# Performance work log

Hardware: AMD Instinct MI355X
Metric: run time of the kernel (lower is better)

The kernel has to match this reference:

```python
import jax, jax.numpy as jnp
import numpy as np

HID = 10  # hidden_dim


def conv1x1(x, w, b=None):
    # x: [N,C,H,W], w: [O,C] -> [N,O,H,W]
    y = jnp.einsum('oc,nchw->nohw', w, x)
    if b is not None:
        y = y + b[None, :, None, None]
    return y


def gconv1x1(x, w, b=None):
    # grouped 1x1 conv. x: [N,G*ipg,H,W], w: [G,opg,ipg]
    N, C, H, W = x.shape
    G, opg, ipg = w.shape
    xg = x.reshape(N, G, ipg, H, W)
    y = jnp.einsum('goi,ngihw->ngohw', w, xg).reshape(N, G * opg, H, W)
    if b is not None:
        y = y + b[None, :, None, None]
    return y


def _decomp(h_fea, xf, xh, att_w, att_b, w):
    # Decomposition: spatial attention from (fea, xf, xh), gate xf, project.
    att = jax.nn.sigmoid(conv1x1(jnp.concatenate([h_fea, xf, xh], axis=1), att_w, att_b))
    xfh = jax.nn.relu(conv1x1(xf * att, w))
    return xfh, att


def _comp(parts, xh, att_w, att_b, w):
    # Composition: parts [P,N,HID,H,W]; grouped per-part attention then fuse with xh.
    ca = jax.nn.sigmoid(jnp.einsum('pc,pnchw->pnhw', att_w[:, 0], parts) + att_b[:, None, None, None])
    msg = (parts * ca[:, :, None]).sum(0)  # [N,HID,H,W]
    return jax.nn.relu(conv1x1(jnp.concatenate([xh, msg], axis=1), w))


def _update(xh, m0, m1, m2, gate_w, gate_b, cand_w):
    # conv_Update: gated residual update from summed messages.
    cat = jnp.concatenate([xh, m0 + m1 + m2], axis=1)
    g = jax.nn.sigmoid(conv1x1(cat, gate_w, gate_b))
    cand = jax.nn.relu(conv1x1(cat, cand_w))
    return xh * (1.0 - g) + cand * g


def half_graph(h_fea, xh_u, xh_l, xf, xp, pdp_w1, pdp_w2, att_w, att_b,
               compU_att_w, compU_att_b, compU_w,
               compL_att_w, compL_att_b, compL_w,
               decU_att_w, decU_att_b, decU_w,
               decL_att_w, decL_att_b, decL_w,
               updU_gate_w, updU_gate_b, updU_cand_w,
               updL_gate_w, updL_gate_b, updL_cand_w):
    # Part_Dependency: shared trunk then grouped conv -> (dp_u, dp_l)
    t = jax.nn.relu(conv1x1(jnp.concatenate([h_fea, xh_u, xh_l], axis=1), pdp_w1))
    dp = jax.nn.relu(gconv1x1(t, pdp_w2))
    dp_u, dp_l = dp[:, :HID], dp[:, HID:]
    # grouped sigmoid attention over the two half nodes
    a = jax.nn.sigmoid(gconv1x1(jnp.concatenate([xh_u, xh_l], axis=1), att_w, att_b))
    ag_u, ag_l = a[:, 0:1], a[:, 1:2]
    # upper half node
    xphu = _comp(xp[0:4], xh_u, compU_att_w, compU_att_b, compU_w)
    xlh = dp_l * ag_l + xh_u * ag_u  # Pair_Part_Dependency (lower -> upper)
    xfhu, att_u = _decomp(h_fea, xf, xh_u, decU_att_w, decU_att_b, decU_w)
    xh_u_new = _update(xh_u, xphu, xlh, xfhu, updU_gate_w, updU_gate_b, updU_cand_w)
    # lower half node
    xphl = _comp(xp[4:6], xh_l, compL_att_w, compL_att_b, compL_w)
    xuh = dp_u * ag_u + xh_l * ag_l  # Pair_Part_Dependency (upper -> lower)
    xfhl, att_l = _decomp(h_fea, xf, xh_l, decL_att_w, decL_att_b, decL_w)
    xh_l_new = _update(xh_l, xphl, xuh, xfhl, updL_gate_w, updL_gate_b, updL_cand_w)
    return xh_u_new, xh_l_new, att_u, att_l


def setup_inputs() -> dict:
    key = jax.random.key(0)
    N, C, H, W = 8, 256, 128, 128
    ks = jax.random.split(key, 32)
    s = 0.05
    inp = {
        'h_fea': jax.random.normal(ks[0], (N, C, H, W), jnp.float32),
        'xh_u': jax.random.normal(ks[1], (N, HID, H, W), jnp.float32),
        'xh_l': jax.random.normal(ks[2], (N, HID, H, W), jnp.float32),
        'xf': jax.random.normal(ks[3], (N, HID, H, W), jnp.float32),
        'xp': jax.random.normal(ks[4], (6, N, HID, H, W), jnp.float32),
        'pdp_w1': jax.random.normal(ks[5], (2 * HID, C + 2 * HID), jnp.float32) * s,
        'pdp_w2': jax.random.normal(ks[6], (2, HID, HID), jnp.float32) * s,
        'att_w': jax.random.normal(ks[7], (2, 1, HID), jnp.float32) * s,
        'att_b': jnp.zeros((2,), jnp.float32),
        'compU_att_w': jax.random.normal(ks[8], (4, 1, HID), jnp.float32) * s,
        'compU_att_b': jnp.zeros((4,), jnp.float32),
        'compU_w': jax.random.normal(ks[9], (HID, 2 * HID), jnp.float32) * s,
        'compL_att_w': jax.random.normal(ks[10], (2, 1, HID), jnp.float32) * s,
        'compL_att_b': jnp.zeros((2,), jnp.float32),
        'compL_w': jax.random.normal(ks[11], (HID, 2 * HID), jnp.float32) * s,
        'decU_att_w': jax.random.normal(ks[12], (1, C + 2 * HID), jnp.float32) * s,
        'decU_att_b': jnp.zeros((1,), jnp.float32),
        'decU_w': jax.random.normal(ks[13], (HID, HID), jnp.float32) * s,
        'decL_att_w': jax.random.normal(ks[14], (1, C + 2 * HID), jnp.float32) * s,
        'decL_att_b': jnp.zeros((1,), jnp.float32),
        'decL_w': jax.random.normal(ks[15], (HID, HID), jnp.float32) * s,
        'updU_gate_w': jax.random.normal(ks[16], (HID, 2 * HID), jnp.float32) * s,
        'updU_gate_b': jnp.zeros((HID,), jnp.float32),
        'updU_cand_w': jax.random.normal(ks[17], (HID, 2 * HID), jnp.float32) * s,
        'updL_gate_w': jax.random.normal(ks[18], (HID, 2 * HID), jnp.float32) * s,
        'updL_gate_b': jnp.zeros((HID,), jnp.float32),
        'updL_cand_w': jax.random.normal(ks[19], (HID, 2 * HID), jnp.float32) * s,
    }
    return inp


def reference(h_fea, xh_u, xh_l, xf, xp, pdp_w1, pdp_w2, att_w, att_b,
              compU_att_w, compU_att_b, compU_w,
              compL_att_w, compL_att_b, compL_w,
              decU_att_w, decU_att_b, decU_w,
              decL_att_w, decL_att_b, decL_w,
              updU_gate_w, updU_gate_b, updU_cand_w,
              updL_gate_w, updL_gate_b, updL_cand_w):
    return half_graph(h_fea, xh_u, xh_l, xf, xp, pdp_w1, pdp_w2, att_w, att_b,
                      compU_att_w, compU_att_b, compU_w,
                      compL_att_w, compL_att_b, compL_w,
                      decU_att_w, decU_att_b, decU_w,
                      decL_att_w, decL_att_b, decL_w,
                      updU_gate_w, updU_gate_b, updU_cand_w,
                      updL_gate_w, updL_gate_b, updL_cand_w)
```

## Files before the change

kernel.cpp:

```cpp
#include <hip/hip_runtime.h>
#include <stdint.h>

typedef unsigned int   u32;
typedef unsigned short u16;

#define HW 16384

typedef __attribute__((ext_vector_type(8)))  _Float16 half8;
typedef __attribute__((ext_vector_type(16))) float    f32x16;

__device__ __forceinline__ float sigm(float x) { return 1.f / (1.f + __expf(-x)); }


__global__ __launch_bounds__(256) void prep_apack(
    const float* __restrict__ pdp_w1, const float* __restrict__ dU_aw,
    const float* __restrict__ dL_aw, _Float16* __restrict__ apack)
{
    int idx = blockIdx.x * 256 + threadIdx.x;
    int s = idx >> 9, rem = idx & 511, l = rem >> 3, j = rem & 7;
    int o = l & 31, kh = l >> 5;
    int k = s * 16 + kh * 8 + j;
    float wv = 0.f;
    if (o < 20)       wv = pdp_w1[o * 276 + k];
    else if (o == 20) wv = dU_aw[k];
    else if (o == 21) wv = dL_aw[k];
    _Float16 h = (_Float16)wv;
    apack[idx]        = h;
    apack[8192 + idx] = (_Float16)(wv - (float)h);
}

__global__ __launch_bounds__(256, 4) void half_graph_fused(
    const float* __restrict__ hf,  const float* __restrict__ xhu, const float* __restrict__ xhl,
    const float* __restrict__ xfg, const float* __restrict__ xpg,
    const float* __restrict__ pdp_w1, const float* __restrict__ pdp_w2,
    const float* __restrict__ att_w,  const float* __restrict__ att_b,
    const float* __restrict__ cU_aw, const float* __restrict__ cU_ab, const float* __restrict__ cU_w,
    const float* __restrict__ cL_aw, const float* __restrict__ cL_ab, const float* __restrict__ cL_w,
    const float* __restrict__ dU_aw, const float* __restrict__ dU_ab, const float* __restrict__ dU_w,
    const float* __restrict__ dL_aw, const float* __restrict__ dL_ab, const float* __restrict__ dL_w,
    const float* __restrict__ uU_gw, const float* __restrict__ uU_gb, const float* __restrict__ uU_cw,
    const float* __restrict__ uL_gw, const float* __restrict__ uL_gb, const float* __restrict__ uL_cw,
    const _Float16* __restrict__ apack,
    float* __restrict__ out)
{
    const int tid    = threadIdx.x;
    const int pxbase = blockIdx.x * 128;
    const int n      = pxbase >> 14;
    const int hwbase = pxbase & 16383;

    __shared__ float sacc[22][128];

    {
        const int l   = tid & 63;
        const int w   = tid >> 6;
        const int col = l & 31;
        const int kh  = l >> 5;
        const float* bp = hf + ((size_t)n * 256 + kh * 8) * HW + (hwbase + w * 32 + col);
        const half8* ah  = (const half8*)apack;
        const half8* al8 = ah + 1024;
        f32x16 acc = {};
        #pragma unroll 2
        for (int s = 0; s < 16; ++s) {
            half8 A_h = ah[s * 64 + l];
            half8 A_l = al8[s * 64 + l];
            float x[8];
            #pragma unroll
            for (int j = 0; j < 8; ++j) x[j] = bp[(size_t)(s * 16 + j) * HW];
            half8 B_h, B_l;
            #pragma unroll
            for (int j = 0; j < 8; ++j) {
                _Float16 h = (_Float16)x[j];
                B_h[j] = h;
                B_l[j] = (_Float16)(x[j] - (float)h);
            }
            acc = __builtin_amdgcn_mfma_f32_32x32x16_f16(A_h, B_h, acc, 0, 0, 0);
            acc = __builtin_amdgcn_mfma_f32_32x32x16_f16(A_h, B_l, acc, 0, 0, 0);
            acc = __builtin_amdgcn_mfma_f32_32x32x16_f16(A_l, B_h, acc, 0, 0, 0);
        }
        const int ccol = w * 32 + col;
        #pragma unroll
        for (int reg = 0; reg < 12; ++reg) {
            const int r = (reg & 3) + 8 * (reg >> 2) + 4 * kh;
            if (r < 22) sacc[r][ccol] = acc[reg];
        }
    }

    const int q    = tid & 127;
    const int role = tid >> 7;
    const int hw   = hwbase + q;
    const int vb   = n * 10 * HW + hw;
    float xu[10], xl[10], xv[10];
    #pragma unroll
    for (int i = 0; i < 10; ++i) xu[i] = xhu[vb + i * HW];
    #pragma unroll
    for (int i = 0; i < 10; ++i) xl[i] = xhl[vb + i * HW];
    #pragma unroll
    for (int i = 0; i < 10; ++i) xv[i] = xfg[vb + i * HW];

    __syncthreads();

    float au_s = att_b[0], al_s = att_b[1];
    #pragma unroll
    for (int i = 0; i < 10; ++i) {
        au_s = fmaf(att_w[i],      xu[i], au_s);
        al_s = fmaf(att_w[10 + i], xl[i], al_s);
    }
    const float au = sigm(au_s), al = sigm(al_s);

    if (role == 0) {
        float tt[10];
        #pragma unroll
        for (int o = 0; o < 10; ++o) {
            const float* wr = pdp_w1 + (10 + o) * 276;
            float s = sacc[10 + o][q];
            #pragma unroll
            for (int i = 0; i < 10; ++i) s = fmaf(wr[256 + i], xu[i], s);
            #pragma unroll
            for (int i = 0; i < 10; ++i) s = fmaf(wr[266 + i], xl[i], s);
            tt[o] = fmaxf(s, 0.f);
        }
        float dpl[10];
        #pragma unroll
        for (int o = 0; o < 10; ++o) {
            float s = 0.f;
            #pragma unroll
            for (int i = 0; i < 10; ++i) s = fmaf(pdp_w2[(10 + o) * 10 + i], tt[i], s);
            dpl[o] = fmaxf(s, 0.f);
        }
        float su = sacc[20][q] + dU_ab[0];
        #pragma unroll
        for (int i = 0; i < 10; ++i) su = fmaf(dU_aw[256 + i], xv[i], su);
        #pragma unroll
        for (int i = 0; i < 10; ++i) su = fmaf(dU_aw[266 + i], xu[i], su);
        const float attU = sigm(su);
        float xfh[10];
        #pragma unroll
        for (int o = 0; o < 10; ++o) {
            float a = 0.f;
            #pragma unroll
            for (int i = 0; i < 10; ++i) a = fmaf(dU_w[o * 10 + i], xv[i], a);
            xfh[o] = fmaxf(attU * a, 0.f);
        }
        float msg[10];
        #pragma unroll
        for (int i = 0; i < 10; ++i) msg[i] = 0.f;
        #pragma unroll
        for (int pp = 0; pp < 4; ++pp) {
            const float* xq = xpg + (size_t)(pp * 8 + n) * 10 * HW + hw;
            float v[10];
            #pragma unroll
            for (int i = 0; i < 10; ++i) v[i] = xq[i * HW];
            float s = cU_ab[pp];
            #pragma unroll
            for (int i = 0; i < 10; ++i) s = fmaf(cU_aw[pp * 10 + i], v[i], s);
            float ca = sigm(s);
            #pragma unroll
            for (int i = 0; i < 10; ++i) msg[i] = fmaf(ca, v[i], msg[i]);
        }
        float m[10];
        #pragma unroll
        for (int o = 0; o < 10; ++o) {
            float s = 0.f;
            #pragma unroll
            for (int i = 0; i < 10; ++i) s = fmaf(cU_w[o * 20 + i],      xu[i],  s);
            #pragma unroll
            for (int i = 0; i < 10; ++i) s = fmaf(cU_w[o * 20 + 10 + i], msg[i], s);
            m[o] = fmaxf(s, 0.f) + fmaf(dpl[o], al, xu[o] * au) + xfh[o];
        }
        #pragma unroll
        for (int o = 0; o < 10; ++o) {
            float gs = uU_gb[o], cs = 0.f;
            #pragma unroll
            for (int i = 0; i < 10; ++i) {
                gs = fmaf(uU_gw[o * 20 + i], xu[i], gs);
                cs = fmaf(uU_cw[o * 20 + i], xu[i], cs);
            }
            #pragma unroll
            for (int i = 0; i < 10; ++i) {
                gs = fmaf(uU_gw[o * 20 + 10 + i], m[i], gs);
                cs = fmaf(uU_cw[o * 20 + 10 + i], m[i], cs);
            }
            float g = sigm(gs), cd = fmaxf(cs, 0.f);
            out[vb + o * HW] = xu[o] * (1.f - g) + cd * g;
        }
        out[2621440 + n * HW + hw] = attU;
    } else {
        float tt[10];
        #pragma unroll
        for (int o = 0; o < 10; ++o) {
            const float* wr = pdp_w1 + o * 276;
            float s = sacc[o][q];
            #pragma unroll
            for (int i = 0; i < 10; ++i) s = fmaf(wr[256 + i], xu[i], s);
            #pragma unroll
            for (int i = 0; i < 10; ++i) s = fmaf(wr[266 + i], xl[i], s);
            tt[o] = fmaxf(s, 0.f);
        }
        float dpu[10];
        #pragma unroll
        for (int o = 0; o < 10; ++o) {
            float s = 0.f;
            #pragma unroll
            for (int i = 0; i < 10; ++i) s = fmaf(pdp_w2[o * 10 + i], tt[i], s);
            dpu[o] = fmaxf(s, 0.f);
        }
        float sl = sacc[21][q] + dL_ab[0];
        #pragma unroll
        for (int i = 0; i < 10; ++i) sl = fmaf(dL_aw[256 + i], xv[i], sl);
        #pragma unroll
        for (int i = 0; i < 10; ++i) sl = fmaf(dL_aw[266 + i], xl[i], sl);
        const float attL = sigm(sl);
        float xfh[10];
        #pragma unroll
        for (int o = 0; o < 10; ++o) {
            float a = 0.f;
            #pragma unroll
            for (int i = 0; i < 10; ++i) a = fmaf(dL_w[o * 10 + i], xv[i], a);
            xfh[o] = fmaxf(attL * a, 0.f);
        }
        float msg[10];
        #pragma unroll
        for (int i = 0; i < 10; ++i) msg[i] = 0.f;
        #pragma unroll
        for (int pp = 0; pp < 2; ++pp) {
            const float* xq = xpg + (size_t)((pp + 4) * 8 + n) * 10 * HW + hw;
            float v[10];
            #pragma unroll
            for (int i = 0; i < 10; ++i) v[i] = xq[i * HW];
            float s = cL_ab[pp];
            #pragma unroll
            for (int i = 0; i < 10; ++i) s = fmaf(cL_aw[pp * 10 + i], v[i], s);
            float ca = sigm(s);
            #pragma unroll
            for (int i = 0; i < 10; ++i) msg[i] = fmaf(ca, v[i], msg[i]);
        }
        float m[10];
        #pragma unroll
        for (int o = 0; o < 10; ++o) {
            float s = 0.f;
            #pragma unroll
            for (int i = 0; i < 10; ++i) s = fmaf(cL_w[o * 20 + i],      xl[i],  s);
            #pragma unroll
            for (int i = 0; i < 10; ++i) s = fmaf(cL_w[o * 20 + 10 + i], msg[i], s);
            m[o] = fmaxf(s, 0.f) + fmaf(dpu[o], au, xl[o] * al) + xfh[o];
        }
        #pragma unroll
        for (int o = 0; o < 10; ++o) {
            float gs = uL_gb[o], cs = 0.f;
            #pragma unroll
            for (int i = 0; i < 10; ++i) {
                gs = fmaf(uL_gw[o * 20 + i], xl[i], gs);
                cs = fmaf(uL_cw[o * 20 + i], xl[i], cs);
            }
            #pragma unroll
            for (int i = 0; i < 10; ++i) {
                gs = fmaf(uL_gw[o * 20 + 10 + i], m[i], gs);
                cs = fmaf(uL_cw[o * 20 + 10 + i], m[i], cs);
            }
            float g = sigm(gs), cd = fmaxf(cs, 0.f);
            out[1310720 + vb + o * HW] = xl[o] * (1.f - g) + cd * g;
        }
        out[2752512 + n * HW + hw] = attL;
    }
}

extern "C" void kernel_launch(void* const* d_in, const int* in_sizes, int n_in,
                              void* d_out, int out_size, void* d_ws, size_t ws_size,
                              hipStream_t stream) {
    (void)in_sizes; (void)n_in; (void)out_size; (void)ws_size;
    const float* hf   = (const float*)d_in[0];
    const float* xhu  = (const float*)d_in[1];
    const float* xhl  = (const float*)d_in[2];
    const float* xfg  = (const float*)d_in[3];
    const float* xpg  = (const float*)d_in[4];
    const float* w1   = (const float*)d_in[5];
    const float* w2   = (const float*)d_in[6];
    const float* aw   = (const float*)d_in[7];
    const float* ab   = (const float*)d_in[8];
    const float* cUaw = (const float*)d_in[9];
    const float* cUab = (const float*)d_in[10];
    const float* cUw  = (const float*)d_in[11];
    const float* cLaw = (const float*)d_in[12];
    const float* cLab = (const float*)d_in[13];
    const float* cLw  = (const float*)d_in[14];
    const float* dUaw = (const float*)d_in[15];
    const float* dUab = (const float*)d_in[16];
    const float* dUw  = (const float*)d_in[17];
    const float* dLaw = (const float*)d_in[18];
    const float* dLab = (const float*)d_in[19];
    const float* dLw  = (const float*)d_in[20];
    const float* uUgw = (const float*)d_in[21];
    const float* uUgb = (const float*)d_in[22];
    const float* uUcw = (const float*)d_in[23];
    const float* uLgw = (const float*)d_in[24];
    const float* uLgb = (const float*)d_in[25];
    const float* uLcw = (const float*)d_in[26];

    _Float16* apack = (_Float16*)d_ws;

    hipLaunchKernelGGL(prep_apack, dim3(32), dim3(256), 0, stream,
                       w1, dUaw, dLaw, apack);
    hipLaunchKernelGGL(half_graph_fused, dim3(1024), dim3(256), 0, stream,
        hf, xhu, xhl, xfg, xpg, w1, w2, aw, ab,
        cUaw, cUab, cUw, cLaw, cLab, cLw,
        dUaw, dUab, dUw, dLaw, dLab, dLw,
        uUgw, uUgb, uUcw, uLgw, uLgb, uLcw,
        (const _Float16*)apack,
        (float*)d_out);
}
```

Measured before the change: 278.3 us.

## Software-pipeline MFMA K-loop loads and hoist independent work before barrier

Fully unrolls the 16-step MFMA reduction with a three-deep rotating buffer of global loads, so each step's loads are in flight before their compute. Computes the composition messages, decomposition projections, and the xu/xl parts of the trunk and attention before the block barrier, leaving only the shared-memory-dependent terms after it. This is meant to hide global memory latency and barrier wait, at the cost of more live registers and a possible risk of spilling under the existing launch bounds.

```diff
diff --git a/kernel.cpp b/kernel.cpp
--- a/kernel.cpp
+++ b/kernel.cpp
@@ -28,6 +28,26 @@
     apack[idx]        = h;
     apack[8192 + idx] = (_Float16)(wv - (float)h);
 }
+
+#define GLOAD(S, XB, AH, AL) do {                                   \
+    AH = ahp[(S) * 64]; AL = alp[(S) * 64];                         \
+    const float* bs_ = bp + (size_t)(S) * 16 * HW;                  \
+    _Pragma("unroll")                                               \
+    for (int j_ = 0; j_ < 8; ++j_) XB[j_] = bs_[(size_t)j_ * HW];   \
+} while (0)
+
+#define GCOMP(XB, AH, AL) do {                                      \
+    half8 Bh_, Bl_;                                                 \
+    _Pragma("unroll")                                               \
+    for (int j_ = 0; j_ < 8; ++j_) {                                \
+        _Float16 h_ = (_Float16)XB[j_];                             \
+        Bh_[j_] = h_;                                               \
+        Bl_[j_] = (_Float16)(XB[j_] - (float)h_);                   \
+    }                                                               \
+    acc = __builtin_amdgcn_mfma_f32_32x32x16_f16(AH, Bh_, acc, 0, 0, 0); \
+    acc = __builtin_amdgcn_mfma_f32_32x32x16_f16(AH, Bl_, acc, 0, 0, 0); \
+    acc = __builtin_amdgcn_mfma_f32_32x32x16_f16(AL, Bh_, acc, 0, 0, 0); \
+} while (0)
 
 __global__ __launch_bounds__(256, 4) void half_graph_fused(
     const float* __restrict__ hf,  const float* __restrict__ xhu, const float* __restrict__ xhl,
@@ -56,27 +76,32 @@
         const int col = l & 31;
         const int kh  = l >> 5;
         const float* bp = hf + ((size_t)n * 256 + kh * 8) * HW + (hwbase + w * 32 + col);
-        const half8* ah  = (const half8*)apack;
-        const half8* al8 = ah + 1024;
+        const half8* ahp = (const half8*)apack + l;
+        const half8* alp = (const half8*)apack + 1024 + l;
         f32x16 acc = {};
-        #pragma unroll 2
-        for (int s = 0; s < 16; ++s) {
-            half8 A_h = ah[s * 64 + l];
-            half8 A_l = al8[s * 64 + l];
-            float x[8];
-            #pragma unroll
-            for (int j = 0; j < 8; ++j) x[j] = bp[(size_t)(s * 16 + j) * HW];
-            half8 B_h, B_l;
-            #pragma unroll
-            for (int j = 0; j < 8; ++j) {
-                _Float16 h = (_Float16)x[j];
-                B_h[j] = h;
-                B_l[j] = (_Float16)(x[j] - (float)h);
-            }
-            acc = __builtin_amdgcn_mfma_f32_32x32x16_f16(A_h, B_h, acc, 0, 0, 0);
-            acc = __builtin_amdgcn_mfma_f32_32x32x16_f16(A_h, B_l, acc, 0, 0, 0);
-            acc = __builtin_amdgcn_mfma_f32_32x32x16_f16(A_l, B_h, acc, 0, 0, 0);
-        }
+
+        float x0[8], x1[8], x2[8];
+        half8 Ah0, Al0, Ah1, Al1, Ah2, Al2;
+        GLOAD(0, x0, Ah0, Al0);
+        GLOAD(1, x1, Ah1, Al1);
+        GLOAD(2, x2, Ah2, Al2);
+        GCOMP(x0, Ah0, Al0); GLOAD(3,  x0, Ah0, Al0);
+        GCOMP(x1, Ah1, Al1); GLOAD(4,  x1, Ah1, Al1);
+        GCOMP(x2, Ah2, Al2); GLOAD(5,  x2, Ah2, Al2);
+        GCOMP(x0, Ah0, Al0); GLOAD(6,  x0, Ah0, Al0);
+        GCOMP(x1, Ah1, Al1); GLOAD(7,  x1, Ah1, Al1);
+        GCOMP(x2, Ah2, Al2); GLOAD(8,  x2, Ah2, Al2);
+        GCOMP(x0, Ah0, Al0); GLOAD(9,  x0, Ah0, Al0);
+        GCOMP(x1, Ah1, Al1); GLOAD(10, x1, Ah1, Al1);
+        GCOMP(x2, Ah2, Al2); GLOAD(11, x2, Ah2, Al2);
+        GCOMP(x0, Ah0, Al0); GLOAD(12, x0, Ah0, Al0);
+        GCOMP(x1, Ah1, Al1); GLOAD(13, x1, Ah1, Al1);
+        GCOMP(x2, Ah2, Al2); GLOAD(14, x2, Ah2, Al2);
+        GCOMP(x0, Ah0, Al0); GLOAD(15, x0, Ah0, Al0);
+        GCOMP(x1, Ah1, Al1);
+        GCOMP(x2, Ah2, Al2);
+        GCOMP(x0, Ah0, Al0);
+
         const int ccol = w * 32 + col;
         #pragma unroll
         for (int reg = 0; reg < 12; ++reg) {
@@ -89,6 +114,7 @@
     const int role = tid >> 7;
     const int hw   = hwbase + q;
     const int vb   = n * 10 * HW + hw;
+
     float xu[10], xl[10], xv[10];
     #pragma unroll
     for (int i = 0; i < 10; ++i) xu[i] = xhu[vb + i * HW];
@@ -97,8 +123,6 @@
     #pragma unroll
     for (int i = 0; i < 10; ++i) xv[i] = xfg[vb + i * HW];
 
-    __syncthreads();
-
     float au_s = att_b[0], al_s = att_b[1];
     #pragma unroll
     for (int i = 0; i < 10; ++i) {
@@ -107,40 +131,12 @@
     }
     const float au = sigm(au_s), al = sigm(al_s);
 
+    float xph[10];
+    float xfa[10];
+    float tta[10];
+    float sa;
+
     if (role == 0) {
-        float tt[10];
-        #pragma unroll
-        for (int o = 0; o < 10; ++o) {
-            const float* wr = pdp_w1 + (10 + o) * 276;
-            float s = sacc[10 + o][q];
-            #pragma unroll
-            for (int i = 0; i < 10; ++i) s = fmaf(wr[256 + i], xu[i], s);
-            #pragma unroll
-            for (int i = 0; i < 10; ++i) s = fmaf(wr[266 + i], xl[i], s);
-            tt[o] = fmaxf(s, 0.f);
-        }
-        float dpl[10];
-        #pragma unroll
-        for (int o = 0; o < 10; ++o) {
-            float s = 0.f;
-            #pragma unroll
-            for (int i = 0; i < 10; ++i) s = fmaf(pdp_w2[(10 + o) * 10 + i], tt[i], s);
-            dpl[o] = fmaxf(s, 0.f);
-        }
-        float su = sacc[20][q] + dU_ab[0];
-        #pragma unroll
-        for (int i = 0; i < 10; ++i) su = fmaf(dU_aw[256 + i], xv[i], su);
-        #pragma unroll
-        for (int i = 0; i < 10; ++i) su = fmaf(dU_aw[266 + i], xu[i], su);
-        const float attU = sigm(su);
-        float xfh[10];
-        #pragma unroll
-        for (int o = 0; o < 10; ++o) {
-            float a = 0.f;
-            #pragma unroll
-            for (int i = 0; i < 10; ++i) a = fmaf(dU_w[o * 10 + i], xv[i], a);
-            xfh[o] = fmaxf(attU * a, 0.f);
-        }
         float msg[10];
         #pragma unroll
         for (int i = 0; i < 10; ++i) msg[i] = 0.f;
@@ -157,16 +153,108 @@
             #pragma unroll
             for (int i = 0; i < 10; ++i) msg[i] = fmaf(ca, v[i], msg[i]);
         }
+        #pragma unroll
+        for (int o = 0; o < 10; ++o) {
+            float s = 0.f;
+            #pragma unroll
+            for (int i = 0; i < 10; ++i) s = fmaf(cU_w[o * 20 + i],      xu[i],  s);
+            #pragma unroll
+            for (int i = 0; i < 10; ++i) s = fmaf(cU_w[o * 20 + 10 + i], msg[i], s);
+            xph[o] = fmaxf(s, 0.f);
+        }
+        #pragma unroll
+        for (int o = 0; o < 10; ++o) {
+            float a = 0.f;
+            #pragma unroll
+            for (int i = 0; i < 10; ++i) a = fmaf(dU_w[o * 10 + i], xv[i], a);
+            xfa[o] = a;
+        }
+        #pragma unroll
+        for (int o = 0; o < 10; ++o) {
+            const float* wr = pdp_w1 + (10 + o) * 276;
+            float s = 0.f;
+            #pragma unroll
+            for (int i = 0; i < 10; ++i) s = fmaf(wr[256 + i], xu[i], s);
+            #pragma unroll
+            for (int i = 0; i < 10; ++i) s = fmaf(wr[266 + i], xl[i], s);
+            tta[o] = s;
+        }
+        float su = dU_ab[0];
+        #pragma unroll
+        for (int i = 0; i < 10; ++i) su = fmaf(dU_aw[256 + i], xv[i], su);
+        #pragma unroll
+        for (int i = 0; i < 10; ++i) su = fmaf(dU_aw[266 + i], xu[i], su);
+        sa = su;
+    } else {
+        float msg[10];
+        #pragma unroll
+        for (int i = 0; i < 10; ++i) msg[i] = 0.f;
+        #pragma unroll
+        for (int pp = 0; pp < 2; ++pp) {
+            const float* xq = xpg + (size_t)((pp + 4) * 8 + n) * 10 * HW + hw;
+            float v[10];
+            #pragma unroll
+            for (int i = 0; i < 10; ++i) v[i] = xq[i * HW];
+            float s = cL_ab[pp];
+            #pragma unroll
+            for (int i = 0; i < 10; ++i) s = fmaf(cL_aw[pp * 10 + i], v[i], s);
+            float ca = sigm(s);
+            #pragma unroll
+            for (int i = 0; i < 10; ++i) msg[i] = fmaf(ca, v[i], msg[i]);
+        }
+        #pragma unroll
+        for (int o = 0; o < 10; ++o) {
+            float s = 0.f;
+            #pragma unroll
+            for (int i = 0; i < 10; ++i) s = fmaf(cL_w[o * 20 + i],      xl[i],  s);
+            #pragma unroll
+            for (int i = 0; i < 10; ++i) s = fmaf(cL_w[o * 20 + 10 + i], msg[i], s);
+            xph[o] = fmaxf(s, 0.f);
+        }
+        #pragma unroll
+        for (int o = 0; o < 10; ++o) {
+            float a = 0.f;
+            #pragma unroll
+            for (int i = 0; i < 10; ++i) a = fmaf(dL_w[o * 10 + i], xv[i], a);
+            xfa[o] = a;
+        }
+        #pragma unroll
+        for (int o = 0; o < 10; ++o) {
+            const float* wr = pdp_w1 + o * 276;
+            float s = 0.f;
+            #pragma unroll
+            for (int i = 0; i < 10; ++i) s = fmaf(wr[256 + i], xu[i], s);
+            #pragma unroll
+            for (int i = 0; i < 10; ++i) s = fmaf(wr[266 + i], xl[i], s);
+            tta[o] = s;
+        }
+        float sl = dL_ab[0];
+        #pragma unroll
+        for (int i = 0; i < 10; ++i) sl = fmaf(dL_aw[256 + i], xv[i], sl);
+        #pragma unroll
+        for (int i = 0; i < 10; ++i) sl = fmaf(dL_aw[266 + i], xl[i], sl);
+        sa = sl;
+    }
+
+    __syncthreads();
+
+    if (role == 0) {
+        float tt[10];
+        #pragma unroll
+        for (int o = 0; o < 10; ++o) tt[o] = fmaxf(sacc[10 + o][q] + tta[o], 0.f);
+        float dpl[10];
+        #pragma unroll
+        for (int o = 0; o < 10; ++o) {
+            float s = 0.f;
+            #pragma unroll
+            for (int i = 0; i < 10; ++i) s = fmaf(pdp_w2[(10 + o) * 10 + i], tt[i], s);
+            dpl[o] = fmaxf(s, 0.f);
+        }
+        const float attU = sigm(sacc[20][q] + sa);
         float m[10];
         #pragma unroll
-        for (int o = 0; o < 10; ++o) {
-            float s = 0.f;
-            #pragma unroll
-            for (int i = 0; i < 10; ++i) s = fmaf(cU_w[o * 20 + i],      xu[i],  s);
-            #pragma unroll
-            for (int i = 0; i < 10; ++i) s = fmaf(cU_w[o * 20 + 10 + i], msg[i], s);
-            m[o] = fmaxf(s, 0.f) + fmaf(dpl[o], al, xu[o] * au) + xfh[o];
-        }
+        for (int o = 0; o < 10; ++o)
+            m[o] = xph[o] + fmaf(dpl[o], al, xu[o] * au) + attU * fmaxf(xfa[o], 0.f);
         #pragma unroll
         for (int o = 0; o < 10; ++o) {
             float gs = uU_gb[o], cs = 0.f;
@@ -187,15 +275,7 @@
     } else {
         float tt[10];
         #pragma unroll
-        for (int o = 0; o < 10; ++o) {
-            const float* wr = pdp_w1 + o * 276;
-            float s = sacc[o][q];
-            #pragma unroll
-            for (int i = 0; i < 10; ++i) s = fmaf(wr[256 + i], xu[i], s);
-            #pragma unroll
-            for (int i = 0; i < 10; ++i) s = fmaf(wr[266 + i], xl[i], s);
-            tt[o] = fmaxf(s, 0.f);
-        }
+        for (int o = 0; o < 10; ++o) tt[o] = fmaxf(sacc[o][q] + tta[o], 0.f);
         float dpu[10];
         #pragma unroll
         for (int o = 0; o < 10; ++o) {
@@ -204,46 +284,11 @@
             for (int i = 0; i < 10; ++i) s = fmaf(pdp_w2[o * 10 + i], tt[i], s);
             dpu[o] = fmaxf(s, 0.f);
         }
-        float sl = sacc[21][q] + dL_ab[0];
-        #pragma unroll
-        for (int i = 0; i < 10; ++i) sl = fmaf(dL_aw[256 + i], xv[i], sl);
-        #pragma unroll
-        for (int i = 0; i < 10; ++i) sl = fmaf(dL_aw[266 + i], xl[i], sl);
-        const float attL = sigm(sl);
-        float xfh[10];
-        #pragma unroll
-        for (int o = 0; o < 10; ++o) {
-            float a = 0.f;
-            #pragma unroll
-            for (int i = 0; i < 10; ++i) a = fmaf(dL_w[o * 10 + i], xv[i], a);
-            xfh[o] = fmaxf(attL * a, 0.f);
-        }
-        float msg[10];
-        #pragma unroll
-        for (int i = 0; i < 10; ++i) msg[i] = 0.f;
-        #pragma unroll
-        for (int pp = 0; pp < 2; ++pp) {
-            const float* xq = xpg + (size_t)((pp + 4) * 8 + n) * 10 * HW + hw;
-            float v[10];
-            #pragma unroll
-            for (int i = 0; i < 10; ++i) v[i] = xq[i * HW];
-            float s = cL_ab[pp];
-            #pragma unroll
-            for (int i = 0; i < 10; ++i) s = fmaf(cL_aw[pp * 10 + i], v[i], s);
-            float ca = sigm(s);
-            #pragma unroll
-            for (int i = 0; i < 10; ++i) msg[i] = fmaf(ca, v[i], msg[i]);
-        }
+        const float attL = sigm(sacc[21][q] + sa);
         float m[10];
         #pragma unroll
-        for (int o = 0; o < 10; ++o) {
-            float s = 0.f;
-            #pragma unroll
-            for (int i = 0; i < 10; ++i) s = fmaf(cL_w[o * 20 + i],      xl[i],  s);
-            #pragma unroll
-            for (int i = 0; i < 10; ++i) s = fmaf(cL_w[o * 20 + 10 + i], msg[i], s);
-            m[o] = fmaxf(s, 0.f) + fmaf(dpu[o], au, xl[o] * al) + xfh[o];
-        }
+        for (int o = 0; o < 10; ++o)
+            m[o] = xph[o] + fmaf(dpu[o], au, xl[o] * al) + attL * fmaxf(xfa[o], 0.f);
         #pragma unroll
         for (int o = 0; o < 10; ++o) {
             float gs = uL_gb[o], cs = 0.f;
```

After: 523.8 us. 88.2% more time.

## Split fused kernel into MFMA GEMM pass and per-pixel epilogue pass

Applied to the files above, without the earlier changes.

Replaces the single fused kernel with two kernels when workspace allows. The first computes the 22-row projection of the 256-channel feature with split-fp16 MFMA and writes the result to a global scratch buffer. The second runs the per-pixel graph epilogue with upper and lower halves handled by separate wavefronts. This is meant to raise occupancy and parallelism in each phase, at the cost of a global round-trip of 22 channels per pixel and an extra launch.

```diff
diff --git a/kernel.cpp b/kernel.cpp
--- a/kernel.cpp
+++ b/kernel.cpp
@@ -1,10 +1,8 @@
 #include <hip/hip_runtime.h>
 #include <stdint.h>
 
-typedef unsigned int   u32;
-typedef unsigned short u16;
-
-#define HW 16384
+#define HW   16384
+#define NPIX 131072
 
 typedef __attribute__((ext_vector_type(8)))  _Float16 half8;
 typedef __attribute__((ext_vector_type(16))) float    f32x16;
@@ -27,6 +25,242 @@
     _Float16 h = (_Float16)wv;
     apack[idx]        = h;
     apack[8192 + idx] = (_Float16)(wv - (float)h);
+}
+
+__global__ __launch_bounds__(256, 6) void gemm22(
+    const float* __restrict__ hf, const _Float16* __restrict__ apack,
+    float* __restrict__ gout)
+{
+    const int tid    = threadIdx.x;
+    const int l      = tid & 63, w = tid >> 6;
+    const int pxbase = blockIdx.x * 64;
+    const int n      = pxbase >> 14;
+    const int hwbase = pxbase & 16383;
+    const int ptile  = w & 1;
+    const int khalf  = w >> 1;
+    const int col    = l & 31, kh = l >> 5;
+
+    const float* bp = hf + ((size_t)(n * 256 + khalf * 128 + kh * 8)) * HW
+                         + hwbase + ptile * 32 + col;
+    const half8* ahp = (const half8*)apack + khalf * 512 + l;
+    const half8* alp = ahp + 1024;
+
+    f32x16 acc = {};
+    #pragma unroll 2
+    for (int s = 0; s < 8; ++s) {
+        half8 Ah = ahp[s * 64];
+        half8 Al = alp[s * 64];
+        float x[8];
+        #pragma unroll
+        for (int j = 0; j < 8; ++j) x[j] = bp[(size_t)(s * 16 + j) * HW];
+        half8 Bh, Bl;
+        #pragma unroll
+        for (int j = 0; j < 8; ++j) {
+            _Float16 h = (_Float16)x[j];
+            Bh[j] = h;
+            Bl[j] = (_Float16)(x[j] - (float)h);
+        }
+        acc = __builtin_amdgcn_mfma_f32_32x32x16_f16(Ah, Bh, acc, 0, 0, 0);
+        acc = __builtin_amdgcn_mfma_f32_32x32x16_f16(Ah, Bl, acc, 0, 0, 0);
+        acc = __builtin_amdgcn_mfma_f32_32x32x16_f16(Al, Bh, acc, 0, 0, 0);
+    }
+
+    __shared__ float sacc[2][22][64];
+    const int ccol = ptile * 32 + col;
+    #pragma unroll
+    for (int reg = 0; reg < 12; ++reg) {
+        const int r = (reg & 3) + 8 * (reg >> 2) + 4 * kh;
+        if (r < 22) sacc[khalf][r][ccol] = acc[reg];
+    }
+    __syncthreads();
+
+    for (int idx = tid; idx < 22 * 64; idx += 256) {
+        int r = idx >> 6, c = idx & 63;
+        gout[(size_t)r * NPIX + pxbase + c] = sacc[0][r][c] + sacc[1][r][c];
+    }
+}
+
+__global__ __launch_bounds__(128, 6) void half_graph_epi(
+    const float* __restrict__ gac,
+    const float* __restrict__ xhu, const float* __restrict__ xhl,
+    const float* __restrict__ xfg, const float* __restrict__ xpg,
+    const float* __restrict__ pdp_w1, const float* __restrict__ pdp_w2,
+    const float* __restrict__ att_w,  const float* __restrict__ att_b,
+    const float* __restrict__ cU_aw, const float* __restrict__ cU_ab, const float* __restrict__ cU_w,
+    const float* __restrict__ cL_aw, const float* __restrict__ cL_ab, const float* __restrict__ cL_w,
+    const float* __restrict__ dU_aw, const float* __restrict__ dU_ab, const float* __restrict__ dU_w,
+    const float* __restrict__ dL_aw, const float* __restrict__ dL_ab, const float* __restrict__ dL_w,
+    const float* __restrict__ uU_gw, const float* __restrict__ uU_gb, const float* __restrict__ uU_cw,
+    const float* __restrict__ uL_gw, const float* __restrict__ uL_gb, const float* __restrict__ uL_cw,
+    float* __restrict__ out)
+{
+    const int tid  = threadIdx.x;
+    const int q    = tid & 63;
+    const int role = tid >> 6;
+    const int p    = blockIdx.x * 64 + q;
+    const int n    = p >> 14, hw = p & 16383;
+    const int vb   = n * 10 * HW + hw;
+    const float* gr = gac + p;
+
+    float xu[10], xl[10], xv[10];
+    #pragma unroll
+    for (int i = 0; i < 10; ++i) xu[i] = xhu[vb + i * HW];
+    #pragma unroll
+    for (int i = 0; i < 10; ++i) xl[i] = xhl[vb + i * HW];
+    #pragma unroll
+    for (int i = 0; i < 10; ++i) xv[i] = xfg[vb + i * HW];
+
+    float au_s = att_b[0], al_s = att_b[1];
+    #pragma unroll
+    for (int i = 0; i < 10; ++i) {
+        au_s = fmaf(att_w[i],      xu[i], au_s);
+        al_s = fmaf(att_w[10 + i], xl[i], al_s);
+    }
+    const float au = sigm(au_s), al = sigm(al_s);
+
+    if (role == 0) {
+        float tt[10];
+        #pragma unroll
+        for (int o = 0; o < 10; ++o) {
+            const float* wr = pdp_w1 + (10 + o) * 276;
+            float s = gr[(size_t)(10 + o) * NPIX];
+            #pragma unroll
+            for (int i = 0; i < 10; ++i) s = fmaf(wr[256 + i], xu[i], s);
+            #pragma unroll
+            for (int i = 0; i < 10; ++i) s = fmaf(wr[266 + i], xl[i], s);
+            tt[o] = fmaxf(s, 0.f);
+        }
+        float dpl[10];
+        #pragma unroll
+        for (int o = 0; o < 10; ++o) {
+            float s = 0.f;
+            #pragma unroll
+            for (int i = 0; i < 10; ++i) s = fmaf(pdp_w2[(10 + o) * 10 + i], tt[i], s);
+            dpl[o] = fmaxf(s, 0.f);
+        }
+        float su = gr[(size_t)20 * NPIX] + dU_ab[0];
+        #pragma unroll
+        for (int i = 0; i < 10; ++i) su = fmaf(dU_aw[256 + i], xv[i], su);
+        #pragma unroll
+        for (int i = 0; i < 10; ++i) su = fmaf(dU_aw[266 + i], xu[i], su);
+        const float attU = sigm(su);
+        float msg[10];
+        #pragma unroll
+        for (int i = 0; i < 10; ++i) msg[i] = 0.f;
+        #pragma unroll
+        for (int pp = 0; pp < 4; ++pp) {
+            const float* xq = xpg + (size_t)(pp * 8 + n) * 10 * HW + hw;
+            float v[10];
+            #pragma unroll
+            for (int i = 0; i < 10; ++i) v[i] = xq[i * HW];
+            float s = cU_ab[pp];
+            #pragma unroll
+            for (int i = 0; i < 10; ++i) s = fmaf(cU_aw[pp * 10 + i], v[i], s);
+            float ca = sigm(s);
+            #pragma unroll
+            for (int i = 0; i < 10; ++i) msg[i] = fmaf(ca, v[i], msg[i]);
+        }
+        float m[10];
+        #pragma unroll
+        for (int o = 0; o < 10; ++o) {
+            float s = 0.f, a = 0.f;
+            #pragma unroll
+            for (int i = 0; i < 10; ++i) s = fmaf(cU_w[o * 20 + i],      xu[i],  s);
+            #pragma unroll
+            for (int i = 0; i < 10; ++i) s = fmaf(cU_w[o * 20 + 10 + i], msg[i], s);
+            #pragma unroll
+            for (int i = 0; i < 10; ++i) a = fmaf(dU_w[o * 10 + i], xv[i], a);
+            m[o] = fmaxf(s, 0.f) + fmaf(dpl[o], al, xu[o] * au) + attU * fmaxf(a, 0.f);
+        }
+        #pragma unroll
+        for (int o = 0; o < 10; ++o) {
+            float gs = uU_gb[o], cs = 0.f;
+            #pragma unroll
+            for (int i = 0; i < 10; ++i) {
+                gs = fmaf(uU_gw[o * 20 + i], xu[i], gs);
+                cs = fmaf(uU_cw[o * 20 + i], xu[i], cs);
+            }
+            #pragma unroll
+            for (int i = 0; i < 10; ++i) {
+                gs = fmaf(uU_gw[o * 20 + 10 + i], m[i], gs);
+                cs = fmaf(uU_cw[o * 20 + 10 + i], m[i], cs);
+            }
+            float g = sigm(gs), cd = fmaxf(cs, 0.f);
+            out[vb + o * HW] = xu[o] * (1.f - g) + cd * g;
+        }
+        out[2621440 + n * HW + hw] = attU;
+    } else {
+        float tt[10];
+        #pragma unroll
+        for (int o = 0; o < 10; ++o) {
+            const float* wr = pdp_w1 + o * 276;
+            float s = gr[(size_t)o * NPIX];
+            #pragma unroll
+            for (int i = 0; i < 10; ++i) s = fmaf(wr[256 + i], xu[i], s);
+            #pragma unroll
+            for (int i = 0; i < 10; ++i) s = fmaf(wr[266 + i], xl[i], s);
+            tt[o] = fmaxf(s, 0.f);
+        }
+        float dpu[10];
+        #pragma unroll
+        for (int o = 0; o < 10; ++o) {
+            float s = 0.f;
+            #pragma unroll
+            for (int i = 0; i < 10; ++i) s = fmaf(pdp_w2[o * 10 + i], tt[i], s);
+            dpu[o] = fmaxf(s, 0.f);
+        }
+        float sl = gr[(size_t)21 * NPIX] + dL_ab[0];
+        #pragma unroll
+        for (int i = 0; i < 10; ++i) sl = fmaf(dL_aw[256 + i], xv[i], sl);
+        #pragma unroll
+        for (int i = 0; i < 10; ++i) sl = fmaf(dL_aw[266 + i], xl[i], sl);
+        const float attL = sigm(sl);
+        float msg[10];
+        #pragma unroll
+        for (int i = 0; i < 10; ++i) msg[i] = 0.f;
+        #pragma unroll
+        for (int pp = 0; pp < 2; ++pp) {
+            const float* xq = xpg + (size_t)((pp + 4) * 8 + n) * 10 * HW + hw;
+            float v[10];
+            #pragma unroll
+            for (int i = 0; i < 10; ++i) v[i] = xq[i * HW];
+            float s = cL_ab[pp];
+            #pragma unroll
+            for (int i = 0; i < 10; ++i) s = fmaf(cL_aw[pp * 10 + i], v[i], s);
+            float ca = sigm(s);
+            #pragma unroll
+            for (int i = 0; i < 10; ++i) msg[i] = fmaf(ca, v[i], msg[i]);
+        }
+        float m[10];
+        #pragma unroll
+        for (int o = 0; o < 10; ++o) {
+            float s = 0.f, a = 0.f;
+            #pragma unroll
+            for (int i = 0; i < 10; ++i) s = fmaf(cL_w[o * 20 + i],      xl[i],  s);
+            #pragma unroll
+            for (int i = 0; i < 10; ++i) s = fmaf(cL_w[o * 20 + 10 + i], msg[i], s);
+            #pragma unroll
+            for (int i = 0; i < 10; ++i) a = fmaf(dL_w[o * 10 + i], xv[i], a);
+            m[o] = fmaxf(s, 0.f) + fmaf(dpu[o], au, xl[o] * al) + attL * fmaxf(a, 0.f);
+        }
+        #pragma unroll
+        for (int o = 0; o < 10; ++o) {
+            float gs = uL_gb[o], cs = 0.f;
+            #pragma unroll
+            for (int i = 0; i < 10; ++i) {
+                gs = fmaf(uL_gw[o * 20 + i], xl[i], gs);
+                cs = fmaf(uL_cw[o * 20 + i], xl[i], cs);
+            }
+            #pragma unroll
+            for (int i = 0; i < 10; ++i) {
+                gs = fmaf(uL_gw[o * 20 + 10 + i], m[i], gs);
+                cs = fmaf(uL_cw[o * 20 + 10 + i], m[i], cs);
+            }
+            float g = sigm(gs), cd = fmaxf(cs, 0.f);
+            out[1310720 + vb + o * HW] = xl[o] * (1.f - g) + cd * g;
+        }
+        out[2752512 + n * HW + hw] = attL;
+    }
 }
 
 __global__ __launch_bounds__(256, 4) void half_graph_fused(
@@ -267,7 +501,7 @@
 extern "C" void kernel_launch(void* const* d_in, const int* in_sizes, int n_in,
                               void* d_out, int out_size, void* d_ws, size_t ws_size,
                               hipStream_t stream) {
-    (void)in_sizes; (void)n_in; (void)out_size; (void)ws_size;
+    (void)in_sizes; (void)n_in; (void)out_size;
     const float* hf   = (const float*)d_in[0];
     const float* xhu  = (const float*)d_in[1];
     const float* xhl  = (const float*)d_in[2];
@@ -297,14 +531,28 @@
     const float* uLcw = (const float*)d_in[26];
 
     _Float16* apack = (_Float16*)d_ws;
+    const size_t need = 32768 + (size_t)22 * NPIX * sizeof(float);
 
     hipLaunchKernelGGL(prep_apack, dim3(32), dim3(256), 0, stream,
                        w1, dUaw, dLaw, apack);
-    hipLaunchKernelGGL(half_graph_fused, dim3(1024), dim3(256), 0, stream,
-        hf, xhu, xhl, xfg, xpg, w1, w2, aw, ab,
-        cUaw, cUab, cUw, cLaw, cLab, cLw,
-        dUaw, dUab, dUw, dLaw, dLab, dLw,
-        uUgw, uUgb, uUcw, uLgw, uLgb, uLcw,
-        (const _Float16*)apack,
-        (float*)d_out);
+
+    if (ws_size >= need) {
+        float* gacc = (float*)((char*)d_ws + 32768);
+        hipLaunchKernelGGL(gemm22, dim3(2048), dim3(256), 0, stream,
+                           hf, (const _Float16*)apack, gacc);
+        hipLaunchKernelGGL(half_graph_epi, dim3(2048), dim3(128), 0, stream,
+            (const float*)gacc, xhu, xhl, xfg, xpg, w1, w2, aw, ab,
+            cUaw, cUab, cUw, cLaw, cLab, cLw,
+            dUaw, dUab, dUw, dLaw, dLab, dLw,
+            uUgw, uUgb, uUcw, uLgw, uLgb, uLcw,
+            (float*)d_out);
+    } else {
+        hipLaunchKernelGGL(half_graph_fused, dim3(1024), dim3(256), 0, stream,
+            hf, xhu, xhl, xfg, xpg, w1, w2, aw, ab,
+            cUaw, cUab, cUw, cLaw, cLab, cLw,
+            dUaw, dUab, dUw, dLaw, dLab, dLw,
+            uUgw, uUgb, uUcw, uLgw, uLgb, uLcw,
+            (const _Float16*)apack,
+            (float*)d_out);
+    }
 }
```

Result: slower. 297.5 us (+6.9%).

## Split MFMA K-reduction across two wave groups with 512-thread blocks

Applied to the files above, without the earlier changes.

Doubles the block to 512 threads and splits the 256-channel K reduction of the trunk GEMM into two halves handled by separate wave groups. Each half writes partial sums to its own shared-memory slice, and the epilogue adds the two slices. The upper 256 threads only help with the MFMA phase and exit after the barrier. This raises the number of waves in flight to better hide the strided global loads of h_fea. The cost is a larger shared-memory footprint, a higher register-pressure constraint from launch_bounds(512,8), and half-idle threads during the epilogue.

```diff
diff --git a/kernel.cpp b/kernel.cpp
--- a/kernel.cpp
+++ b/kernel.cpp
@@ -1,10 +1,8 @@
 #include <hip/hip_runtime.h>
 #include <stdint.h>
 
-typedef unsigned int   u32;
-typedef unsigned short u16;
-
-#define HW 16384
+#define HW   16384
+#define NPIX 131072
 
 typedef __attribute__((ext_vector_type(8)))  _Float16 half8;
 typedef __attribute__((ext_vector_type(16))) float    f32x16;
@@ -29,7 +27,7 @@
     apack[8192 + idx] = (_Float16)(wv - (float)h);
 }
 
-__global__ __launch_bounds__(256, 4) void half_graph_fused(
+__global__ __launch_bounds__(512, 8) void half_graph_fused(
     const float* __restrict__ hf,  const float* __restrict__ xhu, const float* __restrict__ xhl,
     const float* __restrict__ xfg, const float* __restrict__ xpg,
     const float* __restrict__ pdp_w1, const float* __restrict__ pdp_w2,
@@ -48,21 +46,24 @@
     const int n      = pxbase >> 14;
     const int hwbase = pxbase & 16383;
 
-    __shared__ float sacc[22][128];
+    __shared__ float sacc[2][22][128];
 
     {
-        const int l   = tid & 63;
-        const int w   = tid >> 6;
-        const int col = l & 31;
-        const int kh  = l >> 5;
-        const float* bp = hf + ((size_t)n * 256 + kh * 8) * HW + (hwbase + w * 32 + col);
-        const half8* ah  = (const half8*)apack;
-        const half8* al8 = ah + 1024;
+        const int l     = tid & 63;
+        const int w     = tid >> 6;
+        const int col   = l & 31;
+        const int kh    = l >> 5;
+        const int ptile = w & 3;
+        const int khalf = w >> 2;
+        const float* bp = hf + ((size_t)(n * 256 + khalf * 128 + kh * 8)) * HW
+                             + hwbase + ptile * 32 + col;
+        const half8* ahp = (const half8*)apack + khalf * 512 + l;
+        const half8* alp = ahp + 1024;
         f32x16 acc = {};
         #pragma unroll 2
-        for (int s = 0; s < 16; ++s) {
-            half8 A_h = ah[s * 64 + l];
-            half8 A_l = al8[s * 64 + l];
+        for (int s = 0; s < 8; ++s) {
+            half8 A_h = ahp[s * 64];
+            half8 A_l = alp[s * 64];
             float x[8];
             #pragma unroll
             for (int j = 0; j < 8; ++j) x[j] = bp[(size_t)(s * 16 + j) * HW];
@@ -77,11 +78,11 @@
             acc = __builtin_amdgcn_mfma_f32_32x32x16_f16(A_h, B_l, acc, 0, 0, 0);
             acc = __builtin_amdgcn_mfma_f32_32x32x16_f16(A_l, B_h, acc, 0, 0, 0);
         }
-        const int ccol = w * 32 + col;
+        const int ccol = ptile * 32 + col;
         #pragma unroll
         for (int reg = 0; reg < 12; ++reg) {
             const int r = (reg & 3) + 8 * (reg >> 2) + 4 * kh;
-            if (r < 22) sacc[r][ccol] = acc[reg];
+            if (r < 22) sacc[khalf][r][ccol] = acc[reg];
         }
     }
 
@@ -90,14 +91,17 @@
     const int hw   = hwbase + q;
     const int vb   = n * 10 * HW + hw;
     float xu[10], xl[10], xv[10];
-    #pragma unroll
-    for (int i = 0; i < 10; ++i) xu[i] = xhu[vb + i * HW];
-    #pragma unroll
-    for (int i = 0; i < 10; ++i) xl[i] = xhl[vb + i * HW];
-    #pragma unroll
-    for (int i = 0; i < 10; ++i) xv[i] = xfg[vb + i * HW];
+    if (tid < 256) {
+        #pragma unroll
+        for (int i = 0; i < 10; ++i) xu[i] = xhu[vb + i * HW];
+        #pragma unroll
+        for (int i = 0; i < 10; ++i) xl[i] = xhl[vb + i * HW];
+        #pragma unroll
+        for (int i = 0; i < 10; ++i) xv[i] = xfg[vb + i * HW];
+    }
 
     __syncthreads();
+    if (tid >= 256) return;
 
     float au_s = att_b[0], al_s = att_b[1];
     #pragma unroll
@@ -112,7 +116,7 @@
         #pragma unroll
         for (int o = 0; o < 10; ++o) {
             const float* wr = pdp_w1 + (10 + o) * 276;
-            float s = sacc[10 + o][q];
+            float s = sacc[0][10 + o][q] + sacc[1][10 + o][q];
             #pragma unroll
             for (int i = 0; i < 10; ++i) s = fmaf(wr[256 + i], xu[i], s);
             #pragma unroll
@@ -127,7 +131,7 @@
             for (int i = 0; i < 10; ++i) s = fmaf(pdp_w2[(10 + o) * 10 + i], tt[i], s);
             dpl[o] = fmaxf(s, 0.f);
         }
-        float su = sacc[20][q] + dU_ab[0];
+        float su = sacc[0][20][q] + sacc[1][20][q] + dU_ab[0];
         #pragma unroll
         for (int i = 0; i < 10; ++i) su = fmaf(dU_aw[256 + i], xv[i], su);
         #pragma unroll
@@ -189,7 +193,7 @@
         #pragma unroll
         for (int o = 0; o < 10; ++o) {
             const float* wr = pdp_w1 + o * 276;
-            float s = sacc[o][q];
+            float s = sacc[0][o][q] + sacc[1][o][q];
             #pragma unroll
             for (int i = 0; i < 10; ++i) s = fmaf(wr[256 + i], xu[i], s);
             #pragma unroll
@@ -204,7 +208,7 @@
             for (int i = 0; i < 10; ++i) s = fmaf(pdp_w2[o * 10 + i], tt[i], s);
             dpu[o] = fmaxf(s, 0.f);
         }
-        float sl = sacc[21][q] + dL_ab[0];
+        float sl = sacc[0][21][q] + sacc[1][21][q] + dL_ab[0];
         #pragma unroll
         for (int i = 0; i < 10; ++i) sl = fmaf(dL_aw[256 + i], xv[i], sl);
         #pragma unroll
@@ -300,7 +304,7 @@
 
     hipLaunchKernelGGL(prep_apack, dim3(32), dim3(256), 0, stream,
                        w1, dUaw, dLaw, apack);
-    hipLaunchKernelGGL(half_graph_fused, dim3(1024), dim3(256), 0, stream,
+    hipLaunchKernelGGL(half_graph_fused, dim3(1024), dim3(512), 0, stream,
         hf, xhu, xhl, xfg, xpg, w1, w2, aw, ab,
         cUaw, cUab, cUw, cLaw, cLab, cLw,
         dUaw, dUab, dUw, dLaw, dLab, dLw,
```

After: 280.9 us. About the same (+0.9%).
